# Kernel tuning notes

Measured on AMD Instinct MI355X. Metric: run time of the kernel, lower is better.

Reference implementation:

```python
import jax, jax.numpy as jnp
import numpy as np

EPS = 1e-12


def agnn_layer(x, row, col, num_nodes):
    """AGNN propagation with beta frozen at 1.0 (requires_grad=False in source).
    alpha_ij = softmax_{j in N(i)} ( beta * cos(x_i, x_j) ); out_i = sum_j alpha_ij * x_j.
    row = destination node of each edge (segment id), col = source node.
    """
    xn = x / (jnp.linalg.norm(x, axis=-1, keepdims=True) + EPS)  # unit-norm features
    score = jnp.sum(xn[row] * xn[col], axis=-1)                   # [E] beta=1 * cos sim
    smax = jax.ops.segment_max(score, row, num_segments=num_nodes)
    e = jnp.exp(score - smax[row])                                # stable softmax numerator
    denom = jax.ops.segment_sum(e, row, num_segments=num_nodes)
    alpha = e / jnp.maximum(denom[row], EPS)                      # [E]
    out = jax.ops.segment_sum(alpha[:, None] * x[col], row, num_segments=num_nodes)
    return out


def setup_inputs() -> dict:
    key = jax.random.key(0)
    ks = jax.random.split(key, 8)
    N, E = 100000, 1600000
    IN_DIM, HID, OUT_DIM = 128, 64, 64
    x = jax.random.normal(ks[0], (N, IN_DIM), dtype=jnp.float32)
    edge_row = jnp.sort(jax.random.randint(ks[1], (E,), 0, N))
    edge_col = jax.random.randint(ks[2], (E,), 0, N)
    # Linear params (PyTorch nn.Linear style: y = x @ W.T + b)
    s1 = 1.0 / np.sqrt(IN_DIM)
    W1 = jax.random.uniform(ks[3], (HID, IN_DIM), jnp.float32, -s1, s1)
    b1 = jax.random.uniform(ks[4], (HID,), jnp.float32, -s1, s1)
    s2 = 1.0 / np.sqrt(HID)
    W2 = jax.random.uniform(ks[5], (OUT_DIM, HID), jnp.float32, -s2, s2)
    b2 = jax.random.uniform(ks[6], (OUT_DIM,), jnp.float32, -s2, s2)
    return {"x": x, "edge_row": edge_row, "edge_col": edge_col,
            "W1": W1, "b1": b1, "W2": W2, "b2": b2}


def reference(x, edge_row, edge_col, W1, b1, W2, b2):
    N = x.shape[0]
    h = jax.nn.relu(x @ W1.T + b1)
    for _ in range(4):  # 4 frozen-beta AGNN layers
        h = jax.nn.relu(agnn_layer(h, edge_row, edge_col, N))
    return h @ W2.T + b2
```

## Files before the change

kernel.cpp:

```cpp
#include <hip/hip_runtime.h>


typedef _Float16 h2 __attribute__((ext_vector_type(2)));

union U4H { uint4 u; h2 h[4]; };
union U2H { uint2 u; h2 h[2]; };
union UHI { unsigned u; h2 h; };

#define DEV_INLINE __device__ __forceinline__

DEV_INLINE h2 mkh2(float a, float b) {
    h2 r; r.x = (_Float16)a; r.y = (_Float16)b; return r;
}

__global__ __launch_bounds__(256) void build_rowptr(const int* __restrict__ row,
                                                    int* __restrict__ ptr,
                                                    int N, int E) {
    int i = blockIdx.x * blockDim.x + threadIdx.x;
    if (i > N) return;
    int lo = 0, hi = E;
    while (lo < hi) {
        int mid = (lo + hi) >> 1;
        if (row[mid] < i) lo = mid + 1; else hi = mid;
    }
    ptr[i] = lo;
}

#define SEG 8192
__global__ __launch_bounds__(1024) void build_perm_seg(const int* __restrict__ ptr,
                                                       int* __restrict__ perm,
                                                       int N) {
    __shared__ int a[1024], b[1024];
    const int t    = threadIdx.x;
    const int base = blockIdx.x * SEG;
    const int end  = (base + SEG < N) ? base + SEG : N;

    a[t] = 0;
    __syncthreads();
    for (int i = base + t; i < end; i += 1024) {
        int d = ptr[i + 1] - ptr[i];
        if (d > 1023) d = 1023;
        atomicAdd(&a[d], 1);
    }
    __syncthreads();

    const int h = a[t];
    int* src = a; int* dst = b;
    for (int off = 1; off < 1024; off <<= 1) {
        int v = src[t] + (t >= off ? src[t - off] : 0);
        dst[t] = v;
        __syncthreads();
        int* tmp = src; src = dst; dst = tmp;
    }
    src[t] = src[t] - h;
    __syncthreads();

    for (int i = base + t; i < end; i += 1024) {
        int d = ptr[i + 1] - ptr[i];
        if (d > 1023) d = 1023;
        int pos = base + atomicAdd(&src[d], 1);
        perm[pos] = i;
    }
}

__global__ __launch_bounds__(256) void gemm1_relu(const float* __restrict__ x,
                                                  const float* __restrict__ W1,
                                                  const float* __restrict__ b1,
                                                  unsigned short* __restrict__ xn,
                                                  float* __restrict__ nrm,
                                                  int N) {
    __shared__ __align__(16) float Wt[32 * 64];
    __shared__ __align__(16) float xT[32 * 64];
    const int tid  = threadIdx.x;
    const int tx   = tid & 15;
    const int ty   = tid >> 4;
    const int base = blockIdx.x * 64;

    float4 b4 = ((const float4*)b1)[tx];
    float4 acc[4];
    acc[0] = b4; acc[1] = b4; acc[2] = b4; acc[3] = b4;

    for (int kc = 0; kc < 128; kc += 32) {
        if (kc) __syncthreads();
        const float4* W4 = (const float4*)W1;
        for (int idx = tid; idx < 32 * 16; idx += 256) {
            int o = idx & 63, k4 = idx >> 6;
            float4 v = W4[o * 32 + (kc >> 2) + k4];
            Wt[(4 * k4 + 0) * 64 + o] = v.x;
            Wt[(4 * k4 + 1) * 64 + o] = v.y;
            Wt[(4 * k4 + 2) * 64 + o] = v.z;
            Wt[(4 * k4 + 3) * 64 + o] = v.w;
        }
        const float4* x4p = (const float4*)x;
        for (int idx = tid; idx < 32 * 16; idx += 256) {
            int mm = idx & 63, k4 = idx >> 6;
            int node = base + mm;
            float4 v = make_float4(0.f, 0.f, 0.f, 0.f);
            if (node < N) v = x4p[(size_t)node * 32 + (kc >> 2) + k4];
            xT[(4 * k4 + 0) * 64 + mm] = v.x;
            xT[(4 * k4 + 1) * 64 + mm] = v.y;
            xT[(4 * k4 + 2) * 64 + mm] = v.z;
            xT[(4 * k4 + 3) * 64 + mm] = v.w;
        }
        __syncthreads();

#pragma unroll 4
        for (int k = 0; k < 32; ++k) {
            const float4 w4 = *(const float4*)&Wt[k * 64 + 4 * tx];
            const float4 xv = *(const float4*)&xT[k * 64 + 4 * ty];
            acc[0].x = fmaf(xv.x, w4.x, acc[0].x);
            acc[0].y = fmaf(xv.x, w4.y, acc[0].y);
            acc[0].z = fmaf(xv.x, w4.z, acc[0].z);
            acc[0].w = fmaf(xv.x, w4.w, acc[0].w);
            acc[1].x = fmaf(xv.y, w4.x, acc[1].x);
            acc[1].y = fmaf(xv.y, w4.y, acc[1].y);
            acc[1].z = fmaf(xv.y, w4.z, acc[1].z);
            acc[1].w = fmaf(xv.y, w4.w, acc[1].w);
            acc[2].x = fmaf(xv.z, w4.x, acc[2].x);
            acc[2].y = fmaf(xv.z, w4.y, acc[2].y);
            acc[2].z = fmaf(xv.z, w4.z, acc[2].z);
            acc[2].w = fmaf(xv.z, w4.w, acc[2].w);
            acc[3].x = fmaf(xv.w, w4.x, acc[3].x);
            acc[3].y = fmaf(xv.w, w4.y, acc[3].y);
            acc[3].z = fmaf(xv.w, w4.z, acc[3].z);
            acc[3].w = fmaf(xv.w, w4.w, acc[3].w);
        }
    }

#pragma unroll
    for (int mm = 0; mm < 4; ++mm) {
        float4 r = acc[mm];
        r.x = fmaxf(r.x, 0.f); r.y = fmaxf(r.y, 0.f);
        r.z = fmaxf(r.z, 0.f); r.w = fmaxf(r.w, 0.f);
        float s = fmaf(r.x, r.x, fmaf(r.y, r.y, fmaf(r.z, r.z, r.w * r.w)));
        s += __shfl_xor(s, 1, 64);
        s += __shfl_xor(s, 2, 64);
        s += __shfl_xor(s, 4, 64);
        s += __shfl_xor(s, 8, 64);
        const float nn  = sqrtf(s) + 1e-12f;
        const float inv = 1.f / nn;
        int node = base + 4 * ty + mm;
        if (node < N) {
            U2H pk;
            pk.h[0] = mkh2(r.x * inv, r.y * inv);
            pk.h[1] = mkh2(r.z * inv, r.w * inv);
            *(uint2*)&xn[(size_t)node * 64 + 4 * tx] = pk.u;
            if (tx == mm) nrm[node] = nn;
        }
    }
}

__global__ __launch_bounds__(256) void agnn_layer(const uint4* __restrict__ xn4,
                                                  const float* __restrict__ nrm,
                                                  const int* __restrict__ ptr,
                                                  const int* __restrict__ col,
                                                  const int* __restrict__ perm,
                                                  uint4* __restrict__ xo4,
                                                  float* __restrict__ nrmo,
                                                  int N) {
    const int tid  = threadIdx.x;
    const int lane = tid & 63;
    const int g    = (lane >> 3) & 1;
    const int sub  = lane & 7;
    const int slot = blockIdx.x * 16 + (tid >> 4);
    if (slot >= N) return;
    const int i = perm[slot];

    U4H hi_;
    hi_.u = xn4[(unsigned)i * 8u + sub];
    {
        const _Float16 L2E = (_Float16)1.4426950408889634f;
        h2 l2 = {L2E, L2E};
#pragma unroll
        for (int t = 0; t < 4; ++t) hi_.h[t] *= l2;
    }

    const int p0 = ptr[i], p1 = ptr[i + 1];

    float den = 0.f;
    U4H acc;
    acc.h[0] = mkh2(0.f, 0.f); acc.h[1] = mkh2(0.f, 0.f);
    acc.h[2] = mkh2(0.f, 0.f); acc.h[3] = mkh2(0.f, 0.f);

#define EDGE_BODY(VU, NRMJ)                                                  \
    {                                                                        \
        U4H xa; xa.u = (VU);                                                 \
        float s = 0.f;                                                       \
        s = __builtin_amdgcn_fdot2(hi_.h[0], xa.h[0], s, false);             \
        s = __builtin_amdgcn_fdot2(hi_.h[1], xa.h[1], s, false);             \
        s = __builtin_amdgcn_fdot2(hi_.h[2], xa.h[2], s, false);             \
        s = __builtin_amdgcn_fdot2(hi_.h[3], xa.h[3], s, false);             \
        s += __shfl_xor(s, 1, 64);                                           \
        s += __shfl_xor(s, 2, 64);                                           \
        s += __shfl_xor(s, 4, 64);                                           \
        const float p = exp2f(s);                                            \
        den += p;                                                            \
        const _Float16 wh = (_Float16)(p * (NRMJ));                          \
        h2 w2 = {wh, wh};                                                    \
        acc.h[0] += w2 * xa.h[0];                                            \
        acc.h[1] += w2 * xa.h[1];                                            \
        acc.h[2] += w2 * xa.h[2];                                            \
        acc.h[3] += w2 * xa.h[3];                                            \
    }

    int e = p0 + g;
    for (; e + 2 < p1; e += 4) {
        const int ja = col[e];
        const int jb = col[e + 2];
        const uint4 va = xn4[(unsigned)ja * 8u + sub];
        const uint4 vb = xn4[(unsigned)jb * 8u + sub];
        const float na = nrm[ja];
        const float nb = nrm[jb];
        EDGE_BODY(va, na)
        EDGE_BODY(vb, nb)
    }
    if (e < p1) {
        const int j = col[e];
        const uint4 v = xn4[(unsigned)j * 8u + sub];
        const float nj = nrm[j];
        EDGE_BODY(v, nj)
    }
#undef EDGE_BODY

    {
        den += __shfl_xor(den, 8, 64);
#pragma unroll
        for (int t = 0; t < 4; ++t) {
            UHI a; a.h = acc.h[t];
            UHI b; b.u = (unsigned)__shfl_xor((int)a.u, 8, 64);
            acc.h[t] = a.h + b.h;
        }
    }

    const float id = 1.f / fmaxf(den, 1e-12f);
    float o[8];
#pragma unroll
    for (int t = 0; t < 4; ++t) {
        o[2 * t]     = fmaxf((float)acc.h[t].x * id, 0.f);
        o[2 * t + 1] = fmaxf((float)acc.h[t].y * id, 0.f);
    }

    float s2 = 0.f;
#pragma unroll
    for (int t = 0; t < 8; ++t) s2 = fmaf(o[t], o[t], s2);
    s2 += __shfl_xor(s2, 1, 64);
    s2 += __shfl_xor(s2, 2, 64);
    s2 += __shfl_xor(s2, 4, 64);
    const float nn  = sqrtf(s2) + 1e-12f;
    const float inv = 1.f / nn;

    if (g == 0) {
        U4H ov;
        ov.h[0] = mkh2(o[0] * inv, o[1] * inv);
        ov.h[1] = mkh2(o[2] * inv, o[3] * inv);
        ov.h[2] = mkh2(o[4] * inv, o[5] * inv);
        ov.h[3] = mkh2(o[6] * inv, o[7] * inv);
        xo4[(unsigned)i * 8u + sub] = ov.u;
        if (sub == 0) nrmo[i] = nn;
    }
}

__global__ __launch_bounds__(256) void gemm2(const unsigned short* __restrict__ xn,
                                             const float* __restrict__ nrm,
                                             const float* __restrict__ W2,
                                             const float* __restrict__ b2,
                                             float* __restrict__ out,
                                             int N) {
    __shared__ __align__(16) float Wt[64 * 64];
    __shared__ __align__(16) float xT[64 * 64];
    const int tid  = threadIdx.x;
    const int tx   = tid & 15;
    const int ty   = tid >> 4;
    const int base = blockIdx.x * 64;

    {
        const float4* W4 = (const float4*)W2;
        for (int idx = tid; idx < 64 * 16; idx += 256) {
            int o = idx & 63, k4 = idx >> 6;
            float4 v = W4[o * 16 + k4];
            Wt[(4 * k4 + 0) * 64 + o] = v.x;
            Wt[(4 * k4 + 1) * 64 + o] = v.y;
            Wt[(4 * k4 + 2) * 64 + o] = v.z;
            Wt[(4 * k4 + 3) * 64 + o] = v.w;
        }
        const uint2* x2 = (const uint2*)xn;
        for (int idx = tid; idx < 64 * 16; idx += 256) {
            int mm = idx & 63, k4 = idx >> 6;
            int node = base + mm;
            U2H v; v.u = make_uint2(0u, 0u);
            float nn = 0.f;
            if (node < N) { v.u = x2[(size_t)node * 16 + k4]; nn = nrm[node]; }
            xT[(4 * k4 + 0) * 64 + mm] = (float)v.h[0].x * nn;
            xT[(4 * k4 + 1) * 64 + mm] = (float)v.h[0].y * nn;
            xT[(4 * k4 + 2) * 64 + mm] = (float)v.h[1].x * nn;
            xT[(4 * k4 + 3) * 64 + mm] = (float)v.h[1].y * nn;
        }
    }
    __syncthreads();

    float4 b4 = ((const float4*)b2)[tx];
    float4 acc[4];
    acc[0] = b4; acc[1] = b4; acc[2] = b4; acc[3] = b4;

#pragma unroll 4
    for (int k = 0; k < 64; ++k) {
        const float4 w4 = *(const float4*)&Wt[k * 64 + 4 * tx];
        const float4 xv = *(const float4*)&xT[k * 64 + 4 * ty];
        acc[0].x = fmaf(xv.x, w4.x, acc[0].x);
        acc[0].y = fmaf(xv.x, w4.y, acc[0].y);
        acc[0].z = fmaf(xv.x, w4.z, acc[0].z);
        acc[0].w = fmaf(xv.x, w4.w, acc[0].w);
        acc[1].x = fmaf(xv.y, w4.x, acc[1].x);
        acc[1].y = fmaf(xv.y, w4.y, acc[1].y);
        acc[1].z = fmaf(xv.y, w4.z, acc[1].z);
        acc[1].w = fmaf(xv.y, w4.w, acc[1].w);
        acc[2].x = fmaf(xv.z, w4.x, acc[2].x);
        acc[2].y = fmaf(xv.z, w4.y, acc[2].y);
        acc[2].z = fmaf(xv.z, w4.z, acc[2].z);
        acc[2].w = fmaf(xv.z, w4.w, acc[2].w);
        acc[3].x = fmaf(xv.w, w4.x, acc[3].x);
        acc[3].y = fmaf(xv.w, w4.y, acc[3].y);
        acc[3].z = fmaf(xv.w, w4.z, acc[3].z);
        acc[3].w = fmaf(xv.w, w4.w, acc[3].w);
    }

#pragma unroll
    for (int mm = 0; mm < 4; ++mm) {
        int node = base + 4 * ty + mm;
        if (node < N) *(float4*)&out[(size_t)node * 64 + 4 * tx] = acc[mm];
    }
}

extern "C" void kernel_launch(void* const* d_in, const int* in_sizes, int n_in,
                              void* d_out, int out_size, void* d_ws, size_t ws_size,
                              hipStream_t stream) {
    const float* x   = (const float*)d_in[0];
    const int*   row = (const int*)d_in[1];
    const int*   col = (const int*)d_in[2];
    const float* W1  = (const float*)d_in[3];
    const float* b1  = (const float*)d_in[4];
    const float* W2  = (const float*)d_in[5];
    const float* b2  = (const float*)d_in[6];
    float* out = (float*)d_out;

    const int N = in_sizes[0] / 128;
    const int E = in_sizes[1];

    char* ws = (char*)d_ws;
    size_t off = 0;
    unsigned short* ha = (unsigned short*)(ws + off); off += (size_t)N * 64 * 2;
    unsigned short* hb = (unsigned short*)(ws + off); off += (size_t)N * 64 * 2;
    float* na_  = (float*)(ws + off); off += (size_t)N * sizeof(float);
    float* nb_  = (float*)(ws + off); off += (size_t)N * sizeof(float);
    int*   ptr  = (int*)  (ws + off); off += (size_t)(N + 1) * sizeof(int);
    off = (off + 15) & ~(size_t)15;
    int*   perm = (int*)  (ws + off); off += (size_t)N * sizeof(int);
    (void)ws_size; (void)n_in; (void)out_size;

    build_rowptr<<<(N + 256) / 256, 256, 0, stream>>>(row, ptr, N, E);

    build_perm_seg<<<(N + SEG - 1) / SEG, 1024, 0, stream>>>(ptr, perm, N);

    const int nbG = (N + 63) / 64;
    gemm1_relu<<<nbG, 256, 0, stream>>>(x, W1, b1, ha, na_, N);

    const int nb16 = (N + 15) / 16;
    unsigned short* hc = ha; unsigned short* hn = hb;
    float* nc = na_; float* nn = nb_;
    for (int l = 0; l < 4; ++l) {
        agnn_layer<<<nb16, 256, 0, stream>>>((const uint4*)hc, nc, ptr, col, perm,
                                             (uint4*)hn, nn, N);
        unsigned short* t = hc; hc = hn; hn = t;
        float* tf = nc; nc = nn; nn = tf;
    }

    gemm2<<<nbG, 256, 0, stream>>>(hc, nc, W2, b2, out, N);
}
```

Measured before the change: 299.1 us.

## Build rowptr by edge scan, shrink perm segments, and double GEMM row tiles

Replaces the per-node binary search for row pointers with a per-edge boundary scan that writes pointer entries where the sorted row id changes. The degree-sorting permutation now uses 1024-node segments with a 256-bin histogram, which gives many more blocks and a cheaper scan. Both dense GEMM kernels now compute 128 nodes per block, so each thread holds 8 accumulators and shared weight tiles are reused across twice as many rows. The trade-offs are higher register and LDS use in the GEMMs and coarser degree binning for the permutation.

```diff
diff --git a/kernel.cpp b/kernel.cpp
--- a/kernel.cpp
+++ b/kernel.cpp
@@ -13,53 +13,54 @@
     h2 r; r.x = (_Float16)a; r.y = (_Float16)b; return r;
 }
 
-__global__ __launch_bounds__(256) void build_rowptr(const int* __restrict__ row,
-                                                    int* __restrict__ ptr,
-                                                    int N, int E) {
-    int i = blockIdx.x * blockDim.x + threadIdx.x;
-    if (i > N) return;
-    int lo = 0, hi = E;
-    while (lo < hi) {
-        int mid = (lo + hi) >> 1;
-        if (row[mid] < i) lo = mid + 1; else hi = mid;
-    }
-    ptr[i] = lo;
-}
-
-#define SEG 8192
+__global__ __launch_bounds__(256) void build_rowptr_scan(const int* __restrict__ row,
+                                                         int* __restrict__ ptr,
+                                                         int N, int E) {
+    int e = blockIdx.x * blockDim.x + threadIdx.x;
+    if (e >= E) return;
+    const int r1 = row[e];
+    const int r0 = (e == 0) ? -1 : row[e - 1];
+    for (int i = r0 + 1; i <= r1; ++i) ptr[i] = e;
+    if (e == E - 1) {
+        for (int i = r1 + 1; i <= N; ++i) ptr[i] = E;
+    }
+}
+
+#define PSEG 1024
 __global__ __launch_bounds__(1024) void build_perm_seg(const int* __restrict__ ptr,
                                                        int* __restrict__ perm,
                                                        int N) {
-    __shared__ int a[1024], b[1024];
+    __shared__ int hist[256];
+    __shared__ int tmp[256];
     const int t    = threadIdx.x;
-    const int base = blockIdx.x * SEG;
-    const int end  = (base + SEG < N) ? base + SEG : N;
-
-    a[t] = 0;
+    const int base = blockIdx.x * PSEG;
+    const int end  = (base + PSEG < N) ? base + PSEG : N;
+    const int cnt  = end - base;
+
+    if (t < 256) hist[t] = 0;
     __syncthreads();
-    for (int i = base + t; i < end; i += 1024) {
-        int d = ptr[i + 1] - ptr[i];
-        if (d > 1023) d = 1023;
-        atomicAdd(&a[d], 1);
+
+    int d = -1;
+    if (t < cnt) {
+        d = ptr[base + t + 1] - ptr[base + t];
+        if (d > 255) d = 255;
+        atomicAdd(&hist[d], 1);
     }
     __syncthreads();
 
-    const int h = a[t];
-    int* src = a; int* dst = b;
-    for (int off = 1; off < 1024; off <<= 1) {
-        int v = src[t] + (t >= off ? src[t - off] : 0);
-        dst[t] = v;
+    int h0 = (t < 256) ? hist[t] : 0;
+    int* src = hist; int* dst = tmp;
+    for (int off = 1; off < 256; off <<= 1) {
+        if (t < 256) dst[t] = src[t] + (t >= off ? src[t - off] : 0);
         __syncthreads();
-        int* tmp = src; src = dst; dst = tmp;
-    }
-    src[t] = src[t] - h;
+        int* tt = src; src = dst; dst = tt;
+    }
+    if (t < 256) src[t] -= h0;
     __syncthreads();
 
-    for (int i = base + t; i < end; i += 1024) {
-        int d = ptr[i + 1] - ptr[i];
-        if (d > 1023) d = 1023;
+    if (t < cnt) {
         int pos = base + atomicAdd(&src[d], 1);
-        perm[pos] = i;
+        perm[pos] = base + t;
     }
 }
 
@@ -70,20 +71,23 @@
                                                   float* __restrict__ nrm,
                                                   int N) {
     __shared__ __align__(16) float Wt[32 * 64];
-    __shared__ __align__(16) float xT[32 * 64];
+    __shared__ __align__(16) float xT[32 * 128];
     const int tid  = threadIdx.x;
     const int tx   = tid & 15;
     const int ty   = tid >> 4;
-    const int base = blockIdx.x * 64;
+    const int base = blockIdx.x * 128;
 
     float4 b4 = ((const float4*)b1)[tx];
-    float4 acc[4];
-    acc[0] = b4; acc[1] = b4; acc[2] = b4; acc[3] = b4;
+    float4 acc[8];
+#pragma unroll
+    for (int mm = 0; mm < 8; ++mm) acc[mm] = b4;
 
     for (int kc = 0; kc < 128; kc += 32) {
         if (kc) __syncthreads();
         const float4* W4 = (const float4*)W1;
-        for (int idx = tid; idx < 32 * 16; idx += 256) {
+#pragma unroll
+        for (int it = 0; it < 2; ++it) {
+            int idx = tid + it * 256;
             int o = idx & 63, k4 = idx >> 6;
             float4 v = W4[o * 32 + (kc >> 2) + k4];
             Wt[(4 * k4 + 0) * 64 + o] = v.x;
@@ -92,43 +96,62 @@
             Wt[(4 * k4 + 3) * 64 + o] = v.w;
         }
         const float4* x4p = (const float4*)x;
-        for (int idx = tid; idx < 32 * 16; idx += 256) {
-            int mm = idx & 63, k4 = idx >> 6;
+#pragma unroll
+        for (int it = 0; it < 4; ++it) {
+            int idx = tid + it * 256;
+            int mm = idx & 127, k4 = idx >> 7;
             int node = base + mm;
             float4 v = make_float4(0.f, 0.f, 0.f, 0.f);
             if (node < N) v = x4p[(size_t)node * 32 + (kc >> 2) + k4];
-            xT[(4 * k4 + 0) * 64 + mm] = v.x;
-            xT[(4 * k4 + 1) * 64 + mm] = v.y;
-            xT[(4 * k4 + 2) * 64 + mm] = v.z;
-            xT[(4 * k4 + 3) * 64 + mm] = v.w;
+            xT[(4 * k4 + 0) * 128 + mm] = v.x;
+            xT[(4 * k4 + 1) * 128 + mm] = v.y;
+            xT[(4 * k4 + 2) * 128 + mm] = v.z;
+            xT[(4 * k4 + 3) * 128 + mm] = v.w;
         }
         __syncthreads();
 
 #pragma unroll 4
         for (int k = 0; k < 32; ++k) {
-            const float4 w4 = *(const float4*)&Wt[k * 64 + 4 * tx];
-            const float4 xv = *(const float4*)&xT[k * 64 + 4 * ty];
-            acc[0].x = fmaf(xv.x, w4.x, acc[0].x);
-            acc[0].y = fmaf(xv.x, w4.y, acc[0].y);
-            acc[0].z = fmaf(xv.x, w4.z, acc[0].z);
-            acc[0].w = fmaf(xv.x, w4.w, acc[0].w);
-            acc[1].x = fmaf(xv.y, w4.x, acc[1].x);
-            acc[1].y = fmaf(xv.y, w4.y, acc[1].y);
-            acc[1].z = fmaf(xv.y, w4.z, acc[1].z);
-            acc[1].w = fmaf(xv.y, w4.w, acc[1].w);
-            acc[2].x = fmaf(xv.z, w4.x, acc[2].x);
-            acc[2].y = fmaf(xv.z, w4.y, acc[2].y);
-            acc[2].z = fmaf(xv.z, w4.z, acc[2].z);
-            acc[2].w = fmaf(xv.z, w4.w, acc[2].w);
-            acc[3].x = fmaf(xv.w, w4.x, acc[3].x);
-            acc[3].y = fmaf(xv.w, w4.y, acc[3].y);
-            acc[3].z = fmaf(xv.w, w4.z, acc[3].z);
-            acc[3].w = fmaf(xv.w, w4.w, acc[3].w);
-        }
-    }
-
-#pragma unroll
-    for (int mm = 0; mm < 4; ++mm) {
+            const float4 w4  = *(const float4*)&Wt[k * 64 + 4 * tx];
+            const float4 xa  = *(const float4*)&xT[k * 128 + 8 * ty];
+            const float4 xb  = *(const float4*)&xT[k * 128 + 8 * ty + 4];
+            acc[0].x = fmaf(xa.x, w4.x, acc[0].x);
+            acc[0].y = fmaf(xa.x, w4.y, acc[0].y);
+            acc[0].z = fmaf(xa.x, w4.z, acc[0].z);
+            acc[0].w = fmaf(xa.x, w4.w, acc[0].w);
+            acc[1].x = fmaf(xa.y, w4.x, acc[1].x);
+            acc[1].y = fmaf(xa.y, w4.y, acc[1].y);
+            acc[1].z = fmaf(xa.y, w4.z, acc[1].z);
+            acc[1].w = fmaf(xa.y, w4.w, acc[1].w);
+            acc[2].x = fmaf(xa.z, w4.x, acc[2].x);
+            acc[2].y = fmaf(xa.z, w4.y, acc[2].y);
+            acc[2].z = fmaf(xa.z, w4.z, acc[2].z);
+            acc[2].w = fmaf(xa.z, w4.w, acc[2].w);
+            acc[3].x = fmaf(xa.w, w4.x, acc[3].x);
+            acc[3].y = fmaf(xa.w, w4.y, acc[3].y);
+            acc[3].z = fmaf(xa.w, w4.z, acc[3].z);
+            acc[3].w = fmaf(xa.w, w4.w, acc[3].w);
+            acc[4].x = fmaf(xb.x, w4.x, acc[4].x);
+            acc[4].y = fmaf(xb.x, w4.y, acc[4].y);
+            acc[4].z = fmaf(xb.x, w4.z, acc[4].z);
+            acc[4].w = fmaf(xb.x, w4.w, acc[4].w);
+            acc[5].x = fmaf(xb.y, w4.x, acc[5].x);
+            acc[5].y = fmaf(xb.y, w4.y, acc[5].y);
+            acc[5].z = fmaf(xb.y, w4.z, acc[5].z);
+            acc[5].w = fmaf(xb.y, w4.w, acc[5].w);
+            acc[6].x = fmaf(xb.z, w4.x, acc[6].x);
+            acc[6].y = fmaf(xb.z, w4.y, acc[6].y);
+            acc[6].z = fmaf(xb.z, w4.z, acc[6].z);
+            acc[6].w = fmaf(xb.z, w4.w, acc[6].w);
+            acc[7].x = fmaf(xb.w, w4.x, acc[7].x);
+            acc[7].y = fmaf(xb.w, w4.y, acc[7].y);
+            acc[7].z = fmaf(xb.w, w4.z, acc[7].z);
+            acc[7].w = fmaf(xb.w, w4.w, acc[7].w);
+        }
+    }
+
+#pragma unroll
+    for (int mm = 0; mm < 8; ++mm) {
         float4 r = acc[mm];
         r.x = fmaxf(r.x, 0.f); r.y = fmaxf(r.y, 0.f);
         r.z = fmaxf(r.z, 0.f); r.w = fmaxf(r.w, 0.f);
@@ -139,7 +162,7 @@
         s += __shfl_xor(s, 8, 64);
         const float nn  = sqrtf(s) + 1e-12f;
         const float inv = 1.f / nn;
-        int node = base + 4 * ty + mm;
+        int node = base + 8 * ty + mm;
         if (node < N) {
             U2H pk;
             pk.h[0] = mkh2(r.x * inv, r.y * inv);
@@ -267,15 +290,17 @@
                                              float* __restrict__ out,
                                              int N) {
     __shared__ __align__(16) float Wt[64 * 64];
-    __shared__ __align__(16) float xT[64 * 64];
+    __shared__ __align__(16) float xT[64 * 128];
     const int tid  = threadIdx.x;
     const int tx   = tid & 15;
     const int ty   = tid >> 4;
-    const int base = blockIdx.x * 64;
+    const int base = blockIdx.x * 128;
 
     {
         const float4* W4 = (const float4*)W2;
-        for (int idx = tid; idx < 64 * 16; idx += 256) {
+#pragma unroll
+        for (int it = 0; it < 4; ++it) {
+            int idx = tid + it * 256;
             int o = idx & 63, k4 = idx >> 6;
             float4 v = W4[o * 16 + k4];
             Wt[(4 * k4 + 0) * 64 + o] = v.x;
@@ -284,49 +309,69 @@
             Wt[(4 * k4 + 3) * 64 + o] = v.w;
         }
         const uint2* x2 = (const uint2*)xn;
-        for (int idx = tid; idx < 64 * 16; idx += 256) {
-            int mm = idx & 63, k4 = idx >> 6;
+#pragma unroll
+        for (int it = 0; it < 8; ++it) {
+            int idx = tid + it * 256;
+            int mm = idx & 127, k4 = idx >> 7;
             int node = base + mm;
             U2H v; v.u = make_uint2(0u, 0u);
             float nn = 0.f;
             if (node < N) { v.u = x2[(size_t)node * 16 + k4]; nn = nrm[node]; }
-            xT[(4 * k4 + 0) * 64 + mm] = (float)v.h[0].x * nn;
-            xT[(4 * k4 + 1) * 64 + mm] = (float)v.h[0].y * nn;
-            xT[(4 * k4 + 2) * 64 + mm] = (float)v.h[1].x * nn;
-            xT[(4 * k4 + 3) * 64 + mm] = (float)v.h[1].y * nn;
+            xT[(4 * k4 + 0) * 128 + mm] = (float)v.h[0].x * nn;
+            xT[(4 * k4 + 1) * 128 + mm] = (float)v.h[0].y * nn;
+            xT[(4 * k4 + 2) * 128 + mm] = (float)v.h[1].x * nn;
+            xT[(4 * k4 + 3) * 128 + mm] = (float)v.h[1].y * nn;
         }
     }
     __syncthreads();
 
     float4 b4 = ((const float4*)b2)[tx];
-    float4 acc[4];
-    acc[0] = b4; acc[1] = b4; acc[2] = b4; acc[3] = b4;
+    float4 acc[8];
+#pragma unroll
+    for (int mm = 0; mm < 8; ++mm) acc[mm] = b4;
 
 #pragma unroll 4
     for (int k = 0; k < 64; ++k) {
-        const float4 w4 = *(const float4*)&Wt[k * 64 + 4 * tx];
-        const float4 xv = *(const float4*)&xT[k * 64 + 4 * ty];
-        acc[0].x = fmaf(xv.x, w4.x, acc[0].x);
-        acc[0].y = fmaf(xv.x, w4.y, acc[0].y);
-        acc[0].z = fmaf(xv.x, w4.z, acc[0].z);
-        acc[0].w = fmaf(xv.x, w4.w, acc[0].w);
-        acc[1].x = fmaf(xv.y, w4.x, acc[1].x);
-        acc[1].y = fmaf(xv.y, w4.y, acc[1].y);
-        acc[1].z = fmaf(xv.y, w4.z, acc[1].z);
-        acc[1].w = fmaf(xv.y, w4.w, acc[1].w);
-        acc[2].x = fmaf(xv.z, w4.x, acc[2].x);
-        acc[2].y = fmaf(xv.z, w4.y, acc[2].y);
-        acc[2].z = fmaf(xv.z, w4.z, acc[2].z);
-        acc[2].w = fmaf(xv.z, w4.w, acc[2].w);
-        acc[3].x = fmaf(xv.w, w4.x, acc[3].x);
-        acc[3].y = fmaf(xv.w, w4.y, acc[3].y);
-        acc[3].z = fmaf(xv.w, w4.z, acc[3].z);
-        acc[3].w = fmaf(xv.w, w4.w, acc[3].w);
-    }
-
-#pragma unroll
-    for (int mm = 0; mm < 4; ++mm) {
-        int node = base + 4 * ty + mm;
+        const float4 w4  = *(const float4*)&Wt[k * 64 + 4 * tx];
+        const float4 xa  = *(const float4*)&xT[k * 128 + 8 * ty];
+        const float4 xb  = *(const float4*)&xT[k * 128 + 8 * ty + 4];
+        acc[0].x = fmaf(xa.x, w4.x, acc[0].x);
+        acc[0].y = fmaf(xa.x, w4.y, acc[0].y);
+        acc[0].z = fmaf(xa.x, w4.z, acc[0].z);
+        acc[0].w = fmaf(xa.x, w4.w, acc[0].w);
+        acc[1].x = fmaf(xa.y, w4.x, acc[1].x);
+        acc[1].y = fmaf(xa.y, w4.y, acc[1].y);
+        acc[1].z = fmaf(xa.y, w4.z, acc[1].z);
+        acc[1].w = fmaf(xa.y, w4.w, acc[1].w);
+        acc[2].x = fmaf(xa.z, w4.x, acc[2].x);
+        acc[2].y = fmaf(xa.z, w4.y, acc[2].y);
+        acc[2].z = fmaf(xa.z, w4.z, acc[2].z);
+        acc[2].w = fmaf(xa.z, w4.w, acc[2].w);
+        acc[3].x = fmaf(xa.w, w4.x, acc[3].x);
+        acc[3].y = fmaf(xa.w, w4.y, acc[3].y);
+        acc[3].z = fmaf(xa.w, w4.z, acc[3].z);
+        acc[3].w = fmaf(xa.w, w4.w, acc[3].w);
+        acc[4].x = fmaf(xb.x, w4.x, acc[4].x);
+        acc[4].y = fmaf(xb.x, w4.y, acc[4].y);
+        acc[4].z = fmaf(xb.x, w4.z, acc[4].z);
+        acc[4].w = fmaf(xb.x, w4.w, acc[4].w);
+        acc[5].x = fmaf(xb.y, w4.x, acc[5].x);
+        acc[5].y = fmaf(xb.y, w4.y, acc[5].y);
+        acc[5].z = fmaf(xb.y, w4.z, acc[5].z);
+        acc[5].w = fmaf(xb.y, w4.w, acc[5].w);
+        acc[6].x = fmaf(xb.z, w4.x, acc[6].x);
+        acc[6].y = fmaf(xb.z, w4.y, acc[6].y);
+        acc[6].z = fmaf(xb.z, w4.z, acc[6].z);
+        acc[6].w = fmaf(xb.z, w4.w, acc[6].w);
+        acc[7].x = fmaf(xb.w, w4.x, acc[7].x);
+        acc[7].y = fmaf(xb.w, w4.y, acc[7].y);
+        acc[7].z = fmaf(xb.w, w4.z, acc[7].z);
+        acc[7].w = fmaf(xb.w, w4.w, acc[7].w);
+    }
+
+#pragma unroll
+    for (int mm = 0; mm < 8; ++mm) {
+        int node = base + 8 * ty + mm;
         if (node < N) *(float4*)&out[(size_t)node * 64 + 4 * tx] = acc[mm];
     }
 }
@@ -357,11 +402,11 @@
     int*   perm = (int*)  (ws + off); off += (size_t)N * sizeof(int);
     (void)ws_size; (void)n_in; (void)out_size;
 
-    build_rowptr<<<(N + 256) / 256, 256, 0, stream>>>(row, ptr, N, E);
-
-    build_perm_seg<<<(N + SEG - 1) / SEG, 1024, 0, stream>>>(ptr, perm, N);
-
-    const int nbG = (N + 63) / 64;
+    build_rowptr_scan<<<(E + 255) / 256, 256, 0, stream>>>(row, ptr, N, E);
+
+    build_perm_seg<<<(N + PSEG - 1) / PSEG, 1024, 0, stream>>>(ptr, perm, N);
+
+    const int nbG = (N + 127) / 128;
     gemm1_relu<<<nbG, 256, 0, stream>>>(x, W1, b1, ha, na_, N);
 
     const int nb16 = (N + 15) / 16;
```

Measured after the change: 304.1 us. About the same (+1.7%).

## Rework preprocessing kernels and enlarge GEMM tiles with register prefetch

Applied to the files above, without the earlier changes.

Replaces the per-node binary-search rowptr build with a per-edge boundary scan, and shrinks the degree-sort segments to 1024 nodes with a 256-bin histogram so more blocks run in parallel. gemm1 now processes 128 nodes per 512-thread block and prefetches the next K-chunk of W1 and x into registers while computing the current one. gemm2 also moves to 128-node tiles with 512 threads. These target the setup and GEMM costs around the AGNN layers, in exchange for more shared memory per block and coarser degree sorting (degrees above 255 share one bin).

```diff
diff --git a/kernel.cpp b/kernel.cpp
--- a/kernel.cpp
+++ b/kernel.cpp
@@ -13,101 +13,122 @@
     h2 r; r.x = (_Float16)a; r.y = (_Float16)b; return r;
 }
 
-__global__ __launch_bounds__(256) void build_rowptr(const int* __restrict__ row,
-                                                    int* __restrict__ ptr,
-                                                    int N, int E) {
-    int i = blockIdx.x * blockDim.x + threadIdx.x;
-    if (i > N) return;
-    int lo = 0, hi = E;
-    while (lo < hi) {
-        int mid = (lo + hi) >> 1;
-        if (row[mid] < i) lo = mid + 1; else hi = mid;
-    }
-    ptr[i] = lo;
-}
-
-#define SEG 8192
+__global__ __launch_bounds__(256) void build_rowptr_scan(const int* __restrict__ row,
+                                                         int* __restrict__ ptr,
+                                                         int N, int E) {
+    int e = blockIdx.x * blockDim.x + threadIdx.x;
+    if (e >= E) return;
+    const int r1 = row[e];
+    const int r0 = (e == 0) ? -1 : row[e - 1];
+    for (int i = r0 + 1; i <= r1; ++i) ptr[i] = e;
+    if (e == E - 1) {
+        for (int i = r1 + 1; i <= N; ++i) ptr[i] = E;
+    }
+}
+
+#define PSEG 1024
 __global__ __launch_bounds__(1024) void build_perm_seg(const int* __restrict__ ptr,
                                                        int* __restrict__ perm,
                                                        int N) {
-    __shared__ int a[1024], b[1024];
+    __shared__ int hist[256];
+    __shared__ int tmp[256];
     const int t    = threadIdx.x;
-    const int base = blockIdx.x * SEG;
-    const int end  = (base + SEG < N) ? base + SEG : N;
-
-    a[t] = 0;
+    const int base = blockIdx.x * PSEG;
+    const int end  = (base + PSEG < N) ? base + PSEG : N;
+    const int cnt  = end - base;
+
+    if (t < 256) hist[t] = 0;
     __syncthreads();
-    for (int i = base + t; i < end; i += 1024) {
-        int d = ptr[i + 1] - ptr[i];
-        if (d > 1023) d = 1023;
-        atomicAdd(&a[d], 1);
+
+    int d = -1;
+    if (t < cnt) {
+        d = ptr[base + t + 1] - ptr[base + t];
+        if (d > 255) d = 255;
+        atomicAdd(&hist[d], 1);
     }
     __syncthreads();
 
-    const int h = a[t];
-    int* src = a; int* dst = b;
-    for (int off = 1; off < 1024; off <<= 1) {
-        int v = src[t] + (t >= off ? src[t - off] : 0);
-        dst[t] = v;
+    int h0 = (t < 256) ? hist[t] : 0;
+    int* src = hist; int* dst = tmp;
+    for (int off = 1; off < 256; off <<= 1) {
+        if (t < 256) dst[t] = src[t] + (t >= off ? src[t - off] : 0);
         __syncthreads();
-        int* tmp = src; src = dst; dst = tmp;
-    }
-    src[t] = src[t] - h;
+        int* tt = src; src = dst; dst = tt;
+    }
+    if (t < 256) src[t] -= h0;
     __syncthreads();
 
-    for (int i = base + t; i < end; i += 1024) {
-        int d = ptr[i + 1] - ptr[i];
-        if (d > 1023) d = 1023;
+    if (t < cnt) {
         int pos = base + atomicAdd(&src[d], 1);
-        perm[pos] = i;
-    }
-}
-
-__global__ __launch_bounds__(256) void gemm1_relu(const float* __restrict__ x,
+        perm[pos] = base + t;
+    }
+}
+
+__global__ __launch_bounds__(512) void gemm1_relu(const float* __restrict__ x,
                                                   const float* __restrict__ W1,
                                                   const float* __restrict__ b1,
                                                   unsigned short* __restrict__ xn,
                                                   float* __restrict__ nrm,
                                                   int N) {
     __shared__ __align__(16) float Wt[32 * 64];
-    __shared__ __align__(16) float xT[32 * 64];
+    __shared__ __align__(16) float xT[32 * 128];
     const int tid  = threadIdx.x;
     const int tx   = tid & 15;
     const int ty   = tid >> 4;
-    const int base = blockIdx.x * 64;
+    const int base = blockIdx.x * 128;
+
+    const float4* W4  = (const float4*)W1;
+    const float4* x4p = (const float4*)x;
+
+    const int wO  = tid & 63;
+    const int wK4 = tid >> 6;
+    const int mA  = tid & 127;
+    const int kA  = tid >> 7;
+    const int mB  = mA;
+    const int kB  = kA + 4;
+    const int nodeA = base + mA;
+
+    float4 wv, xa_, xb_;
+    wv = W4[wO * 32 + wK4];
+    xa_ = make_float4(0.f, 0.f, 0.f, 0.f);
+    xb_ = xa_;
+    if (nodeA < N) {
+        xa_ = x4p[(size_t)nodeA * 32 + kA];
+        xb_ = x4p[(size_t)nodeA * 32 + kB];
+    }
 
     float4 b4 = ((const float4*)b1)[tx];
     float4 acc[4];
     acc[0] = b4; acc[1] = b4; acc[2] = b4; acc[3] = b4;
 
-    for (int kc = 0; kc < 128; kc += 32) {
-        if (kc) __syncthreads();
-        const float4* W4 = (const float4*)W1;
-        for (int idx = tid; idx < 32 * 16; idx += 256) {
-            int o = idx & 63, k4 = idx >> 6;
-            float4 v = W4[o * 32 + (kc >> 2) + k4];
-            Wt[(4 * k4 + 0) * 64 + o] = v.x;
-            Wt[(4 * k4 + 1) * 64 + o] = v.y;
-            Wt[(4 * k4 + 2) * 64 + o] = v.z;
-            Wt[(4 * k4 + 3) * 64 + o] = v.w;
-        }
-        const float4* x4p = (const float4*)x;
-        for (int idx = tid; idx < 32 * 16; idx += 256) {
-            int mm = idx & 63, k4 = idx >> 6;
-            int node = base + mm;
-            float4 v = make_float4(0.f, 0.f, 0.f, 0.f);
-            if (node < N) v = x4p[(size_t)node * 32 + (kc >> 2) + k4];
-            xT[(4 * k4 + 0) * 64 + mm] = v.x;
-            xT[(4 * k4 + 1) * 64 + mm] = v.y;
-            xT[(4 * k4 + 2) * 64 + mm] = v.z;
-            xT[(4 * k4 + 3) * 64 + mm] = v.w;
-        }
+    for (int c = 0; c < 4; ++c) {
+        Wt[(4 * wK4 + 0) * 64 + wO] = wv.x;
+        Wt[(4 * wK4 + 1) * 64 + wO] = wv.y;
+        Wt[(4 * wK4 + 2) * 64 + wO] = wv.z;
+        Wt[(4 * wK4 + 3) * 64 + wO] = wv.w;
+        xT[(4 * kA + 0) * 128 + mA] = xa_.x;
+        xT[(4 * kA + 1) * 128 + mA] = xa_.y;
+        xT[(4 * kA + 2) * 128 + mA] = xa_.z;
+        xT[(4 * kA + 3) * 128 + mA] = xa_.w;
+        xT[(4 * kB + 0) * 128 + mB] = xb_.x;
+        xT[(4 * kB + 1) * 128 + mB] = xb_.y;
+        xT[(4 * kB + 2) * 128 + mB] = xb_.z;
+        xT[(4 * kB + 3) * 128 + mB] = xb_.w;
         __syncthreads();
+
+        if (c < 3) {
+            const int ko = (c + 1) * 8;
+            wv = W4[wO * 32 + ko + wK4];
+            if (nodeA < N) {
+                xa_ = x4p[(size_t)nodeA * 32 + ko + kA];
+                xb_ = x4p[(size_t)nodeA * 32 + ko + kB];
+            }
+        }
 
 #pragma unroll 4
         for (int k = 0; k < 32; ++k) {
             const float4 w4 = *(const float4*)&Wt[k * 64 + 4 * tx];
-            const float4 xv = *(const float4*)&xT[k * 64 + 4 * ty];
+            const float4 xv = *(const float4*)&xT[k * 128 + 4 * ty];
             acc[0].x = fmaf(xv.x, w4.x, acc[0].x);
             acc[0].y = fmaf(xv.x, w4.y, acc[0].y);
             acc[0].z = fmaf(xv.x, w4.z, acc[0].z);
@@ -125,6 +146,7 @@
             acc[3].z = fmaf(xv.w, w4.z, acc[3].z);
             acc[3].w = fmaf(xv.w, w4.w, acc[3].w);
         }
+        if (c < 3) __syncthreads();
     }
 
 #pragma unroll
@@ -260,22 +282,24 @@
     }
 }
 
-__global__ __launch_bounds__(256) void gemm2(const unsigned short* __restrict__ xn,
+__global__ __launch_bounds__(512) void gemm2(const unsigned short* __restrict__ xn,
                                              const float* __restrict__ nrm,
                                              const float* __restrict__ W2,
                                              const float* __restrict__ b2,
                                              float* __restrict__ out,
                                              int N) {
     __shared__ __align__(16) float Wt[64 * 64];
-    __shared__ __align__(16) float xT[64 * 64];
+    __shared__ __align__(16) float xT[64 * 128];
     const int tid  = threadIdx.x;
     const int tx   = tid & 15;
     const int ty   = tid >> 4;
-    const int base = blockIdx.x * 64;
+    const int base = blockIdx.x * 128;
 
     {
         const float4* W4 = (const float4*)W2;
-        for (int idx = tid; idx < 64 * 16; idx += 256) {
+#pragma unroll
+        for (int it = 0; it < 2; ++it) {
+            int idx = tid + it * 512;
             int o = idx & 63, k4 = idx >> 6;
             float4 v = W4[o * 16 + k4];
             Wt[(4 * k4 + 0) * 64 + o] = v.x;
@@ -284,16 +308,18 @@
             Wt[(4 * k4 + 3) * 64 + o] = v.w;
         }
         const uint2* x2 = (const uint2*)xn;
-        for (int idx = tid; idx < 64 * 16; idx += 256) {
-            int mm = idx & 63, k4 = idx >> 6;
+#pragma unroll
+        for (int it = 0; it < 4; ++it) {
+            int idx = tid + it * 512;
+            int mm = idx & 127, k4 = idx >> 7;
             int node = base + mm;
             U2H v; v.u = make_uint2(0u, 0u);
             float nn = 0.f;
             if (node < N) { v.u = x2[(size_t)node * 16 + k4]; nn = nrm[node]; }
-            xT[(4 * k4 + 0) * 64 + mm] = (float)v.h[0].x * nn;
-            xT[(4 * k4 + 1) * 64 + mm] = (float)v.h[0].y * nn;
-            xT[(4 * k4 + 2) * 64 + mm] = (float)v.h[1].x * nn;
-            xT[(4 * k4 + 3) * 64 + mm] = (float)v.h[1].y * nn;
+            xT[(4 * k4 + 0) * 128 + mm] = (float)v.h[0].x * nn;
+            xT[(4 * k4 + 1) * 128 + mm] = (float)v.h[0].y * nn;
+            xT[(4 * k4 + 2) * 128 + mm] = (float)v.h[1].x * nn;
+            xT[(4 * k4 + 3) * 128 + mm] = (float)v.h[1].y * nn;
         }
     }
     __syncthreads();
@@ -305,7 +331,7 @@
 #pragma unroll 4
     for (int k = 0; k < 64; ++k) {
         const float4 w4 = *(const float4*)&Wt[k * 64 + 4 * tx];
-        const float4 xv = *(const float4*)&xT[k * 64 + 4 * ty];
+        const float4 xv = *(const float4*)&xT[k * 128 + 4 * ty];
         acc[0].x = fmaf(xv.x, w4.x, acc[0].x);
         acc[0].y = fmaf(xv.x, w4.y, acc[0].y);
         acc[0].z = fmaf(xv.x, w4.z, acc[0].z);
@@ -357,12 +383,12 @@
     int*   perm = (int*)  (ws + off); off += (size_t)N * sizeof(int);
     (void)ws_size; (void)n_in; (void)out_size;
 
-    build_rowptr<<<(N + 256) / 256, 256, 0, stream>>>(row, ptr, N, E);
-
-    build_perm_seg<<<(N + SEG - 1) / SEG, 1024, 0, stream>>>(ptr, perm, N);
-
-    const int nbG = (N + 63) / 64;
-    gemm1_relu<<<nbG, 256, 0, stream>>>(x, W1, b1, ha, na_, N);
+    build_rowptr_scan<<<(E + 255) / 256, 256, 0, stream>>>(row, ptr, N, E);
+
+    build_perm_seg<<<(N + PSEG - 1) / PSEG, 1024, 0, stream>>>(ptr, perm, N);
+
+    const int nbG = (N + 127) / 128;
+    gemm1_relu<<<nbG, 512, 0, stream>>>(x, W1, b1, ha, na_, N);
 
     const int nb16 = (N + 15) / 16;
     unsigned short* hc = ha; unsigned short* hn = hb;
@@ -374,5 +400,5 @@
         float* tf = nc; nc = nn; nn = tf;
     }
 
-    gemm2<<<nbG, 256, 0, stream>>>(hc, nc, W2, b2, out, N);
-}
+    gemm2<<<nbG, 512, 0, stream>>>(hc, nc, W2, b2, out, N);
+}
```

New measurement: 301.9 us. No clear change (+0.9%).
